# Kernel optimization log

Hardware: AMD Instinct MI355X
Metric: run time of the kernel (lower is better)

Reference implementation:

```python
import jax, jax.numpy as jnp
import numpy as np

B, T, H = 32, 64, 1024  # batch_size, input_number, hidden_size


def _lstm_cell(x, h, c, Wih, Whh, bih, bhh):
    # torch.nn.LSTMCell math: gate order i, f, g, o
    gates = x @ Wih.T + bih + h @ Whh.T + bhh
    i, f, g, o = jnp.split(gates, 4, axis=-1)
    c = jax.nn.sigmoid(f) * c + jax.nn.sigmoid(i) * jnp.tanh(g)
    h = jax.nn.sigmoid(o) * jnp.tanh(c)
    return h, c


def setup_inputs() -> dict:
    key = jax.random.key(0)
    ks = iter(jax.random.split(key, 64))

    def unif(shape, fan):
        s = 1.0 / np.sqrt(fan)
        return jax.random.uniform(next(ks), shape, jnp.float32, -s, s)

    inp = {
        'apperances': jax.random.normal(next(ks), (B, T, 2 * H), jnp.float32),
        'motions': jax.random.normal(next(ks), (B, T, 2 * H), jnp.float32),
    }
    # four LSTM cells: 1a/1m take 2H input, 2a/2m take H input
    for name, in_dim in [('1a', 2 * H), ('2a', H), ('1m', 2 * H), ('2m', H)]:
        inp['Wih_' + name] = unif((4 * H, in_dim), H)
        inp['Whh_' + name] = unif((4 * H, H), H)
        inp['bih_' + name] = unif((4 * H,), H)
        inp['bhh_' + name] = unif((4 * H,), H)
    # two-stream memory fusion (stand-in for MemoryRamTwoStreamModule)
    inp['Wg'] = unif((H, 2 * H), 2 * H)
    inp['bg'] = unif((H,), 2 * H)
    inp['Wa'] = unif((H, H), H)
    inp['ba'] = unif((H,), H)
    inp['Wm'] = unif((H, H), H)
    inp['bm'] = unif((H,), H)
    return inp


def reference(apperances, motions,
              Wih_1a, Whh_1a, bih_1a, bhh_1a,
              Wih_2a, Whh_2a, bih_2a, bhh_2a,
              Wih_1m, Whh_1m, bih_1m, bhh_1m,
              Wih_2m, Whh_2m, bih_2m, bhh_2m,
              Wg, bg, Wa, ba, Wm, bm):
    b, t, _ = apperances.shape
    h = Whh_1a.shape[1]
    xa = jnp.swapaxes(apperances, 0, 1)  # (T, B, 2H)
    xm = jnp.swapaxes(motions, 0, 1)     # (T, B, 2H)
    z = jnp.zeros((b, h), apperances.dtype)

    def step(carry, xs):
        h1a, c1a, h2a, c2a, h1m, c1m, h2m, c2m = carry
        xa_t, xm_t = xs
        h1m, c1m = _lstm_cell(xm_t, h1m, c1m, Wih_1m, Whh_1m, bih_1m, bhh_1m)
        h2m, c2m = _lstm_cell(h1m, h2m, c2m, Wih_2m, Whh_2m, bih_2m, bhh_2m)
        h1a, c1a = _lstm_cell(xa_t, h1a, c1a, Wih_1a, Whh_1a, bih_1a, bhh_1a)
        h2a, c2a = _lstm_cell(h1a, h2a, c2a, Wih_2a, Whh_2a, bih_2a, bhh_2a)
        return (h1a, c1a, h2a, c2a, h1m, c1m, h2m, c2m), (h2a, h2m)

    _, (Ha, Hm) = jax.lax.scan(step, (z, z, z, z, z, z, z, z), (xa, xm))
    Ha = jnp.swapaxes(Ha, 0, 1)  # (B, T, H)
    Hm = jnp.swapaxes(Hm, 0, 1)  # (B, T, H)
    # gated two-stream fusion per timestep (assumed MemoryRamTwoStreamModule)
    g = jax.nn.sigmoid(jnp.einsum('btk,hk->bth', jnp.concatenate([Ha, Hm], -1), Wg) + bg)
    mem = g * jnp.tanh(Ha @ Wa.T + ba) + (1.0 - g) * jnp.tanh(Hm @ Wm.T + bm)
    return mem  # (B, T, H)
```

## Files before the change

### kernel.cpp

```cpp
#include <hip/hip_runtime.h>
#include <cstdint>

typedef _Float16 f16;
typedef _Float16 f16x4v __attribute__((ext_vector_type(4)));
typedef _Float16 f16x8 __attribute__((ext_vector_type(8)));
typedef float f32x4 __attribute__((ext_vector_type(4)));

#define DEV static __device__ __forceinline__

#define GLDS16(gp, lp) __builtin_amdgcn_global_load_lds( \
    (const __attribute__((address_space(1))) void*)(gp), \
    (__attribute__((address_space(3))) void*)(lp), 16, 0, 0)

DEV float sigf(float x) { return 1.0f / (1.0f + __expf(-x)); }
DEV float tanh2(float x) {
  float e = __expf(-2.0f * fabsf(x));
  float t = (1.0f - e) / (1.0f + e);
  return x >= 0.0f ? t : -t;
}

DEV void waitflags(const unsigned* fp, int l) {
  unsigned f;
  do {
    f = __hip_atomic_load(fp + l, __ATOMIC_RELAXED, __HIP_MEMORY_SCOPE_AGENT);
  } while (__any(f == 0));
  asm volatile("" ::: "memory");
  __builtin_amdgcn_sched_barrier(0);
}

__global__ __launch_bounds__(256) void k_cvt_all(
    const float* __restrict__ s0, f16* __restrict__ d0,
    const float* __restrict__ s1, f16* __restrict__ d1,
    const float* __restrict__ s2, f16* __restrict__ d2,
    const float* __restrict__ s3, f16* __restrict__ d3,
    const float* __restrict__ s4, f16* __restrict__ d4,
    const float* __restrict__ s5, f16* __restrict__ d5,
    const float* __restrict__ s6, f16* __restrict__ d6) {
  int bid = blockIdx.x;
  const float* s; f16* d; int base;
  if (bid < 4096)       { s = s0; d = d0; base = bid; }
  else if (bid < 8192)  { s = s1; d = d1; base = bid - 4096; }
  else if (bid < 16384) { s = s2; d = d2; base = bid - 8192; }
  else if (bid < 24576) { s = s3; d = d3; base = bid - 16384; }
  else if (bid < 26624) { s = s4; d = d4; base = bid - 24576; }
  else if (bid < 27648) { s = s5; d = d5; base = bid - 26624; }
  else                  { s = s6; d = d6; base = bid - 27648; }
  int i = (base * 256 + threadIdx.x) * 4;
  float4 v = *(const float4*)(s + i);
  f16x4v o;
  o.x = (f16)v.x; o.y = (f16)v.y; o.z = (f16)v.z; o.w = (f16)v.w;
  *(f16x4v*)(d + i) = o;
}

__global__ __launch_bounds__(256) void k_packw1(const float* __restrict__ Wa,
                                                const float* __restrict__ Wm,
                                                f16* __restrict__ Pa,
                                                f16* __restrict__ Pm) {
  const float* W = blockIdx.y ? Wm : Wa;
  f16* P = blockIdx.y ? Pm : Pa;
  int i2 = blockIdx.x * 256 + threadIdx.x;
  int l = i2 & 63, frag = i2 >> 6;
  int kt = frag & 31, ug = frag >> 5;
  int gate = ug & 3, ut = ug >> 2;
  int row = gate * 1024 + ut * 16 + (l & 15);
  int k = kt * 32 + 8 * (l >> 4);
  const float* s = W + row * 1024 + k;
  f16x8 o;
#pragma unroll
  for (int j = 0; j < 8; ++j) o[j] = (f16)s[j];
  *(f16x8*)(P + frag * 512 + l * 8) = o;
}

__global__ __launch_bounds__(256) void k_packw2(const float* __restrict__ Wiha,
                                                const float* __restrict__ Whha,
                                                const float* __restrict__ Wihm,
                                                const float* __restrict__ Whhm,
                                                f16* __restrict__ Pa,
                                                f16* __restrict__ Pm) {
  const float* Wih = blockIdx.y ? Wihm : Wiha;
  const float* Whh = blockIdx.y ? Whhm : Whha;
  f16* P = blockIdx.y ? Pm : Pa;
  int i2 = blockIdx.x * 256 + threadIdx.x;
  int l = i2 & 63, frag = i2 >> 6;
  int kt = frag & 63, ug = frag >> 6;
  int gate = ug & 3, ut = ug >> 2;
  int row = gate * 1024 + ut * 16 + (l & 15);
  int k = kt * 32 + 8 * (l >> 4);
  const float* s = (k < 1024) ? (Wih + row * 1024 + k)
                              : (Whh + row * 1024 + (k - 1024));
  f16x8 o;
#pragma unroll
  for (int j = 0; j < 8; ++j) o[j] = (f16)s[j];
  *(f16x8*)(P + frag * 512 + l * 8) = o;
}

template <int NKT, int LDA>
__global__ __launch_bounds__(256) void k_igemm(
    const f16* __restrict__ A0, const f16* __restrict__ A1,
    const f16* __restrict__ B0, const f16* __restrict__ B1,
    const float* __restrict__ bi0, const float* __restrict__ bh0,
    const float* __restrict__ bi1, const float* __restrict__ bh1,
    f16* __restrict__ C0, f16* __restrict__ C1) {
  const f16* A = blockIdx.z ? A1 : A0;
  const f16* B = blockIdx.z ? B1 : B0;
  const float* bi = blockIdx.z ? bi1 : bi0;
  const float* bh = blockIdx.z ? bh1 : bh0;
  f16* C = blockIdx.z ? C1 : C0;

  __shared__ alignas(16) f16 As[128 * 64];
  __shared__ alignas(16) f16 Bs[128 * 64];

  int tid = threadIdx.x, l = tid & 63, w = tid >> 6;
  int m0 = blockIdx.x * 128, n0 = blockIdx.y * 128;
  int wm = (w & 1) * 64, wn = (w >> 1) * 64;
  int lr = l & 15, lg = l >> 4;
  int sr = w * 32 + (l >> 3);
  int sc = (l & 7) * 8;

  f32x4 acc[4][4];
  f32x4 zero = {0.f, 0.f, 0.f, 0.f};
#pragma unroll
  for (int mt = 0; mt < 4; ++mt)
#pragma unroll
    for (int nt = 0; nt < 4; ++nt) acc[mt][nt] = zero;

  for (int kt = 0; kt < NKT; ++kt) {
    int k0 = kt * 64;
#pragma unroll
    for (int c2 = 0; c2 < 4; ++c2) {
      GLDS16(A + (size_t)(m0 + sr + c2 * 8) * LDA + k0 + sc, &As[(w * 32 + c2 * 8) * 64]);
      GLDS16(B + (size_t)(n0 + sr + c2 * 8) * LDA + k0 + sc, &Bs[(w * 32 + c2 * 8) * 64]);
    }
    __syncthreads();
#pragma unroll
    for (int ks = 0; ks < 2; ++ks) {
      f16x8 af[4], bf[4];
#pragma unroll
      for (int mt = 0; mt < 4; ++mt)
        af[mt] = *(const f16x8*)&As[(wm + mt * 16 + lr) * 64 + ks * 32 + 8 * lg];
#pragma unroll
      for (int nt = 0; nt < 4; ++nt)
        bf[nt] = *(const f16x8*)&Bs[(wn + nt * 16 + lr) * 64 + ks * 32 + 8 * lg];
#pragma unroll
      for (int mt = 0; mt < 4; ++mt)
#pragma unroll
        for (int nt = 0; nt < 4; ++nt)
          acc[mt][nt] = __builtin_amdgcn_mfma_f32_16x16x32_f16(af[mt], bf[nt], acc[mt][nt], 0, 0, 0);
    }
    __syncthreads();
  }

#pragma unroll
  for (int nt = 0; nt < 4; ++nt) {
    int n = n0 + wn + nt * 16 + lr;
    float bsum = bi[n] + bh[n];
#pragma unroll
    for (int mt = 0; mt < 4; ++mt) {
      int m = m0 + wm + mt * 16 + lg * 4;
#pragma unroll
      for (int r = 0; r < 4; ++r)
        C[(size_t)(m + r) * 4096 + n] = (f16)(acc[mt][nt][r] + bsum);
    }
  }
}

__global__ __launch_bounds__(512, 1) void k_scan2(
    const f16* __restrict__ Wp1_a, const f16* __restrict__ Wp1_m,
    const f16* __restrict__ Wp2_a, const f16* __restrict__ Wp2_m,
    const f16* __restrict__ G_a, const f16* __restrict__ G_m,
    const float* __restrict__ bi2_a, const float* __restrict__ bh2_a,
    const float* __restrict__ bi2_m, const float* __restrict__ bh2_m,
    f16* __restrict__ H1h,
    f16* __restrict__ h2c,
    f16* __restrict__ HaHm,
    unsigned* __restrict__ flags1,
    unsigned* __restrict__ flags2) {
  int bi = blockIdx.x;
  int role = bi >> 7, s = (bi >> 6) & 1, ut = bi & 63, u0 = ut * 16;
  int tid = threadIdx.x, l = tid & 63, w = tid >> 6;
  int lr = l & 15, lg = l >> 4;
  const f16* G = s ? G_m : G_a;
  f16* H1s = H1h + (size_t)s * 64 * 32768;
  f16* h2s = h2c + (size_t)s * 64 * 32768;
  f16* H2o = HaHm + s * 1024;

  f16x8 wreg[8][4];
  if (role == 0) {
    const f16* Wp = s ? Wp1_m : Wp1_a;
#pragma unroll
    for (int ks = 0; ks < 4; ++ks)
#pragma unroll
      for (int g = 0; g < 4; ++g) {
        wreg[ks][g] = *(const f16x8*)(Wp + (size_t)((ut * 4 + g) * 32 + (w * 4 + ks)) * 512 + l * 8);
        asm volatile("" : "+v"(wreg[ks][g]));
      }
  } else {
    const f16* Wp = s ? Wp2_m : Wp2_a;
#pragma unroll
    for (int ks = 0; ks < 8; ++ks)
#pragma unroll
      for (int g = 0; g < 4; ++g) {
        wreg[ks][g] = *(const f16x8*)(Wp + (size_t)((ut * 4 + g) * 64 + (w * 8 + ks)) * 512 + l * 8);
        asm volatile("" : "+v"(wreg[ks][g]));
      }
  }

  __shared__ alignas(16) float red[8][64][33];
  __shared__ alignas(16) f16 Gs[32][4][16];

  int eb = tid >> 4, eu = tid & 15;
  int emt = eb >> 4, elg = (eb >> 2) & 3, er = eb & 3;
  int lred = elg * 16 + eu;
  int idxb = emt * 16 + er;
  float creg = 0.f;
  f32x4 zero = {0.f, 0.f, 0.f, 0.f};

  if (role == 0) {
    int pb = tid >> 4, pg2 = (tid >> 2) & 3, p4 = tid & 3;
    int cb = w * 128;
    for (int t = 0; t < 64; ++t) {
      f16x4v gfrag = *(const f16x4v*)(G + (size_t)(pb * 64 + t) * 4096 + pg2 * 1024 + u0 + p4 * 4);

      f32x4 acc[2][4];
#pragma unroll
      for (int mt = 0; mt < 2; ++mt)
#pragma unroll
        for (int g = 0; g < 4; ++g) acc[mt][g] = zero;

      if (t > 0) {
        if (w == 0) waitflags(flags1 + (size_t)(s * 64 + t - 1) * 64, l);
        __syncthreads();
        const f16* hp = H1s + (size_t)(t - 1) * 32768;
        f16x8 A0[4], A1[4];
#pragma unroll
        for (int ks = 0; ks < 4; ++ks) {
          int col = cb + ks * 32 + 8 * lg;
          A0[ks] = *(const f16x8*)(hp + lr * 1024 + col);
          A1[ks] = *(const f16x8*)(hp + (16 + lr) * 1024 + col);
        }
#pragma unroll
        for (int ks = 0; ks < 4; ++ks)
#pragma unroll
          for (int g = 0; g < 4; ++g) {
            acc[0][g] = __builtin_amdgcn_mfma_f32_16x16x32_f16(A0[ks], wreg[ks][g], acc[0][g], 0, 0, 0);
            acc[1][g] = __builtin_amdgcn_mfma_f32_16x16x32_f16(A1[ks], wreg[ks][g], acc[1][g], 0, 0, 0);
          }
      }

      *(f16x4v*)&Gs[pb][pg2][p4 * 4] = gfrag;
#pragma unroll
      for (int mt = 0; mt < 2; ++mt)
#pragma unroll
        for (int g = 0; g < 4; ++g)
#pragma unroll
          for (int r = 0; r < 4; ++r)
            red[w][l][(mt * 4 + g) * 4 + r] = acc[mt][g][r];
      __syncthreads();

      float pre[4];
#pragma unroll
      for (int g = 0; g < 4; ++g) {
        int idx = idxb + g * 4;
        pre[g] = red[0][lred][idx] + red[1][lred][idx] + red[2][lred][idx] +
                 red[3][lred][idx] + red[4][lred][idx] + red[5][lred][idx] +
                 red[6][lred][idx] + red[7][lred][idx] + (float)Gs[eb][g][eu];
      }
      float cn = sigf(pre[1]) * creg + sigf(pre[0]) * tanh2(pre[2]);
      creg = cn;
      union { unsigned short us; f16 h; } cv;
      cv.h = (f16)(sigf(pre[3]) * tanh2(cn));
      unsigned ov = (unsigned)__shfl_xor((int)(unsigned)cv.us, 1, 64);
      if (!(tid & 1)) {
        unsigned pkv = ((unsigned)cv.us) | (ov << 16);
        __hip_atomic_store((unsigned*)(H1s + (size_t)t * 32768 + eb * 1024 + u0 + eu), pkv,
                           __ATOMIC_RELAXED, __HIP_MEMORY_SCOPE_AGENT);
      }
      asm volatile("s_waitcnt vmcnt(0)" ::: "memory");
      __syncthreads();
      if (tid == 0)
        __hip_atomic_store(flags1 + (size_t)(s * 64 + t) * 64 + ut, 1u,
                           __ATOMIC_RELAXED, __HIP_MEMORY_SCOPE_AGENT);
    }
  } else {
    const float* bip = s ? bi2_m : bi2_a;
    const float* bhp = s ? bh2_m : bh2_a;
    float b2r[4];
#pragma unroll
    for (int g = 0; g < 4; ++g)
      b2r[g] = bip[g * 1024 + u0 + eu] + bhp[g * 1024 + u0 + eu];
    int cb = (w & 3) * 256;

    for (int t = 0; t < 64; ++t) {
      f32x4 acc[2][4];
#pragma unroll
      for (int mt = 0; mt < 2; ++mt)
#pragma unroll
        for (int g = 0; g < 4; ++g) acc[mt][g] = zero;

      if (w == 0) waitflags(flags1 + (size_t)(s * 64 + t) * 64, l);
      if (t > 0 && w == 4) waitflags(flags2 + (size_t)(s * 64 + t - 1) * 64, l);
      __syncthreads();

      if (w < 4) {
        const f16* hp = H1s + (size_t)t * 32768;
        f16x8 A0[4], A1[4], B0[4], B1[4];
#pragma unroll
        for (int ks = 0; ks < 4; ++ks) {
          int c0 = cb + ks * 32 + 8 * lg;
          int c1 = cb + (4 + ks) * 32 + 8 * lg;
          A0[ks] = *(const f16x8*)(hp + lr * 1024 + c0);
          A1[ks] = *(const f16x8*)(hp + (16 + lr) * 1024 + c0);
          B0[ks] = *(const f16x8*)(hp + lr * 1024 + c1);
          B1[ks] = *(const f16x8*)(hp + (16 + lr) * 1024 + c1);
        }
#pragma unroll
        for (int ks = 0; ks < 4; ++ks)
#pragma unroll
          for (int g = 0; g < 4; ++g) {
            acc[0][g] = __builtin_amdgcn_mfma_f32_16x16x32_f16(A0[ks], wreg[ks][g], acc[0][g], 0, 0, 0);
            acc[1][g] = __builtin_amdgcn_mfma_f32_16x16x32_f16(A1[ks], wreg[ks][g], acc[1][g], 0, 0, 0);
          }
#pragma unroll
        for (int ks = 0; ks < 4; ++ks)
#pragma unroll
          for (int g = 0; g < 4; ++g) {
            acc[0][g] = __builtin_amdgcn_mfma_f32_16x16x32_f16(B0[ks], wreg[4 + ks][g], acc[0][g], 0, 0, 0);
            acc[1][g] = __builtin_amdgcn_mfma_f32_16x16x32_f16(B1[ks], wreg[4 + ks][g], acc[1][g], 0, 0, 0);
          }
      } else if (t > 0) {
        const f16* hp = h2s + (size_t)(t - 1) * 32768;
        f16x8 A0[4], A1[4], B0[4], B1[4];
#pragma unroll
        for (int ks = 0; ks < 4; ++ks) {
          int c0 = cb + ks * 32 + 8 * lg;
          int c1 = cb + (4 + ks) * 32 + 8 * lg;
          A0[ks] = *(const f16x8*)(hp + lr * 1024 + c0);
          A1[ks] = *(const f16x8*)(hp + (16 + lr) * 1024 + c0);
          B0[ks] = *(const f16x8*)(hp + lr * 1024 + c1);
          B1[ks] = *(const f16x8*)(hp + (16 + lr) * 1024 + c1);
        }
#pragma unroll
        for (int ks = 0; ks < 4; ++ks)
#pragma unroll
          for (int g = 0; g < 4; ++g) {
            acc[0][g] = __builtin_amdgcn_mfma_f32_16x16x32_f16(A0[ks], wreg[ks][g], acc[0][g], 0, 0, 0);
            acc[1][g] = __builtin_amdgcn_mfma_f32_16x16x32_f16(A1[ks], wreg[ks][g], acc[1][g], 0, 0, 0);
          }
#pragma unroll
        for (int ks = 0; ks < 4; ++ks)
#pragma unroll
          for (int g = 0; g < 4; ++g) {
            acc[0][g] = __builtin_amdgcn_mfma_f32_16x16x32_f16(B0[ks], wreg[4 + ks][g], acc[0][g], 0, 0, 0);
            acc[1][g] = __builtin_amdgcn_mfma_f32_16x16x32_f16(B1[ks], wreg[4 + ks][g], acc[1][g], 0, 0, 0);
          }
      }

#pragma unroll
      for (int mt = 0; mt < 2; ++mt)
#pragma unroll
        for (int g = 0; g < 4; ++g)
#pragma unroll
          for (int r = 0; r < 4; ++r)
            red[w][l][(mt * 4 + g) * 4 + r] = acc[mt][g][r];
      __syncthreads();

      float pre[4];
#pragma unroll
      for (int g = 0; g < 4; ++g) {
        int idx = idxb + g * 4;
        pre[g] = red[0][lred][idx] + red[1][lred][idx] + red[2][lred][idx] +
                 red[3][lred][idx] + red[4][lred][idx] + red[5][lred][idx] +
                 red[6][lred][idx] + red[7][lred][idx] + b2r[g];
      }
      float cn = sigf(pre[1]) * creg + sigf(pre[0]) * tanh2(pre[2]);
      creg = cn;
      union { unsigned short us; f16 h; } cv;
      cv.h = (f16)(sigf(pre[3]) * tanh2(cn));
      unsigned ov = (unsigned)__shfl_xor((int)(unsigned)cv.us, 1, 64);
      if (!(tid & 1)) {
        unsigned pkv = ((unsigned)cv.us) | (ov << 16);
        __hip_atomic_store((unsigned*)(h2s + (size_t)t * 32768 + eb * 1024 + u0 + eu), pkv,
                           __ATOMIC_RELAXED, __HIP_MEMORY_SCOPE_AGENT);
        *(unsigned*)(H2o + (size_t)(eb * 64 + t) * 2048 + u0 + eu) = pkv;
      }
      asm volatile("s_waitcnt vmcnt(0)" ::: "memory");
      __syncthreads();
      if (tid == 0)
        __hip_atomic_store(flags2 + (size_t)(s * 64 + t) * 64 + ut, 1u,
                           __ATOMIC_RELAXED, __HIP_MEMORY_SCOPE_AGENT);
    }
  }
}

DEV void gemm_phase(const f16* __restrict__ H, int kA0,
                    const f16* __restrict__ Bp, int brs, int nk,
                    f16* As, f16* Bs, int m0, int n0, int w, int l,
                    int wm, int wn, f32x4 (&acc)[4][2]) {
  f32x4 zero = {0.f, 0.f, 0.f, 0.f};
#pragma unroll
  for (int mt = 0; mt < 4; ++mt)
#pragma unroll
    for (int nt = 0; nt < 2; ++nt) acc[mt][nt] = zero;
  int lr = l & 15, lg = l >> 4;
  int sc = (l & 7) * 8;
  for (int kt = 0; kt < nk; ++kt) {
    int ka = kA0 + kt * 64, kb = kt * 64;
#pragma unroll
    for (int c2 = 0; c2 < 4; ++c2)
      GLDS16(H + (size_t)(m0 + w * 32 + c2 * 8 + (l >> 3)) * 2048 + ka + sc,
             As + (w * 32 + c2 * 8) * 64);
#pragma unroll
    for (int c2 = 0; c2 < 2; ++c2)
      GLDS16(Bp + (size_t)(n0 + w * 16 + c2 * 8 + (l >> 3)) * brs + kb + sc,
             Bs + (w * 16 + c2 * 8) * 64);
    __syncthreads();
#pragma unroll
    for (int ks = 0; ks < 2; ++ks) {
      f16x8 af[4], bf[2];
#pragma unroll
      for (int mt = 0; mt < 4; ++mt)
        af[mt] = *(const f16x8*)&As[(wm + mt * 16 + lr) * 64 + ks * 32 + 8 * lg];
#pragma unroll
      for (int nt = 0; nt < 2; ++nt)
        bf[nt] = *(const f16x8*)&Bs[(wn + nt * 16 + lr) * 64 + ks * 32 + 8 * lg];
#pragma unroll
      for (int mt = 0; mt < 4; ++mt)
#pragma unroll
        for (int nt = 0; nt < 2; ++nt)
          acc[mt][nt] = __builtin_amdgcn_mfma_f32_16x16x32_f16(af[mt], bf[nt], acc[mt][nt], 0, 0, 0);
    }
    __syncthreads();
  }
}

__global__ __launch_bounds__(256) void k_fusion(
    const f16* __restrict__ H, const f16* __restrict__ Wg16,
    const f16* __restrict__ Wa16, const f16* __restrict__ Wm16,
    const float* __restrict__ bg, const float* __restrict__ ba,
    const float* __restrict__ bm, float* __restrict__ out) {
  __shared__ alignas(16) f16 As[128 * 64];
  __shared__ alignas(16) f16 Bs[64 * 64];
  int tid = threadIdx.x, l = tid & 63, w = tid >> 6;
  int m0 = blockIdx.x * 128, n0 = blockIdx.y * 64;
  int wm = (w & 1) * 64, wn = (w >> 1) * 32;
  int lr = l & 15, lg = l >> 4;

  f32x4 acc[4][2];
  float ta[4][2][4], tm[4][2][4];

  gemm_phase(H, 0, Wa16, 1024, 16, As, Bs, m0, n0, w, l, wm, wn, acc);
#pragma unroll
  for (int nt = 0; nt < 2; ++nt) {
    float bv = ba[n0 + wn + nt * 16 + lr];
#pragma unroll
    for (int mt = 0; mt < 4; ++mt)
#pragma unroll
      for (int r = 0; r < 4; ++r) ta[mt][nt][r] = tanh2(acc[mt][nt][r] + bv);
  }
  gemm_phase(H, 1024, Wm16, 1024, 16, As, Bs, m0, n0, w, l, wm, wn, acc);
#pragma unroll
  for (int nt = 0; nt < 2; ++nt) {
    float bv = bm[n0 + wn + nt * 16 + lr];
#pragma unroll
    for (int mt = 0; mt < 4; ++mt)
#pragma unroll
      for (int r = 0; r < 4; ++r) tm[mt][nt][r] = tanh2(acc[mt][nt][r] + bv);
  }
  gemm_phase(H, 0, Wg16, 2048, 32, As, Bs, m0, n0, w, l, wm, wn, acc);
#pragma unroll
  for (int nt = 0; nt < 2; ++nt) {
    int n = n0 + wn + nt * 16 + lr;
    float bv = bg[n];
#pragma unroll
    for (int mt = 0; mt < 4; ++mt) {
      int m = m0 + wm + mt * 16 + lg * 4;
#pragma unroll
      for (int r = 0; r < 4; ++r) {
        float g = sigf(acc[mt][nt][r] + bv);
        out[(size_t)(m + r) * 1024 + n] = tm[mt][nt][r] + g * (ta[mt][nt][r] - tm[mt][nt][r]);
      }
    }
  }
}

extern "C" void kernel_launch(void* const* d_in, const int* in_sizes, int n_in,
                              void* d_out, int out_size, void* d_ws, size_t ws_size,
                              hipStream_t stream) {
  const float* xa = (const float*)d_in[0];
  const float* xm = (const float*)d_in[1];
  const float* Wih_1a = (const float*)d_in[2];
  const float* Whh_1a = (const float*)d_in[3];
  const float* bih_1a = (const float*)d_in[4];
  const float* bhh_1a = (const float*)d_in[5];
  const float* Wih_2a = (const float*)d_in[6];
  const float* Whh_2a = (const float*)d_in[7];
  const float* bih_2a = (const float*)d_in[8];
  const float* bhh_2a = (const float*)d_in[9];
  const float* Wih_1m = (const float*)d_in[10];
  const float* Whh_1m = (const float*)d_in[11];
  const float* bih_1m = (const float*)d_in[12];
  const float* bhh_1m = (const float*)d_in[13];
  const float* Wih_2m = (const float*)d_in[14];
  const float* Whh_2m = (const float*)d_in[15];
  const float* bih_2m = (const float*)d_in[16];
  const float* bhh_2m = (const float*)d_in[17];
  const float* Wg = (const float*)d_in[18];
  const float* bg = (const float*)d_in[19];
  const float* Wa = (const float*)d_in[20];
  const float* ba = (const float*)d_in[21];
  const float* Wm = (const float*)d_in[22];
  const float* bm = (const float*)d_in[23];

  char* ws = (char*)d_ws;
  const size_t MB = 1024ull * 1024;
  if (ws_size < 138 * MB) return;

  f16* x16a    = (f16*)(ws + 0 * MB);
  f16* x16m    = (f16*)(ws + 8 * MB);
  f16* W1ih16a = (f16*)(ws + 16 * MB);
  f16* W1ih16m = (f16*)(ws + 32 * MB);
  f16* W1p_a   = (f16*)(ws + 48 * MB);
  f16* W1p_m   = (f16*)(ws + 56 * MB);
  f16* W2p_a   = (f16*)(ws + 64 * MB);
  f16* W2p_m   = (f16*)(ws + 80 * MB);
  f16* Wg16    = (f16*)(ws + 96 * MB);
  f16* Wa16    = (f16*)(ws + 100 * MB);
  f16* Wm16    = (f16*)(ws + 102 * MB);
  f16* G0a     = (f16*)(ws + 104 * MB);
  f16* G0m     = (f16*)(ws + 120 * MB);
  unsigned* flags1 = (unsigned*)(ws + 136 * MB);
  unsigned* flags2 = (unsigned*)(ws + 136 * MB + 32768);
  f16* HaHm    = (f16*)(ws + 0 * MB);
  f16* H1h     = (f16*)(ws + 8 * MB);
  f16* h2c     = (f16*)(ws + 16 * MB);

  dim3 B256(256);
  k_cvt_all<<<28672, B256, 0, stream>>>(xa, x16a, xm, x16m, Wih_1a, W1ih16a,
                                        Wih_1m, W1ih16m, Wg, Wg16, Wa, Wa16,
                                        Wm, Wm16);
  k_packw1<<<dim3(2048, 2), B256, 0, stream>>>(Whh_1a, Whh_1m, W1p_a, W1p_m);
  k_packw2<<<dim3(4096, 2), B256, 0, stream>>>(Wih_2a, Whh_2a, Wih_2m, Whh_2m,
                                               W2p_a, W2p_m);
  hipMemsetAsync(flags1, 0, 65536, stream);

  k_igemm<32, 2048><<<dim3(16, 32, 2), B256, 0, stream>>>(
      x16a, x16m, W1ih16a, W1ih16m, bih_1a, bhh_1a, bih_1m, bhh_1m, G0a, G0m);

  k_scan2<<<256, dim3(512), 0, stream>>>(
      W1p_a, W1p_m, W2p_a, W2p_m, G0a, G0m,
      bih_2a, bhh_2a, bih_2m, bhh_2m, H1h, h2c, HaHm, flags1, flags2);

  k_fusion<<<dim3(16, 16), B256, 0, stream>>>(HaHm, Wg16, Wa16, Wm16, bg, ba,
                                              bm, (float*)d_out);
}
```

Baseline: 729.8 us.

## Fuse layer-1 input GEMM into scan kernel with per-timestep readiness counters

Removes the separate input-projection GEMM launch and runs it inside the persistent scan kernel on 128 extra blocks. Those blocks publish per-timestep-pair counters, and the layer-1 scan blocks poll the counters so the recurrence can start before the whole projection is finished. The input is converted and transposed to time-major order so each timestep's rows are contiguous, and the Wih fp32 weights are converted to fp16 on the fly instead of by a separate pass. Layer-2 output is written once to HaHm in time-major order, which drops the duplicate h2 buffer, and the fusion kernel remaps rows on output. The trade-offs are more spin-waiting, a GEMM with smaller tiles that loads fp32 weights directly, and reliance on all 384 blocks being co-resident.

```diff
diff --git a/kernel.cpp b/kernel.cpp
--- a/kernel.cpp
+++ b/kernel.cpp
@@ -28,28 +28,39 @@
   __builtin_amdgcn_sched_barrier(0);
 }
 
+DEV void waitcnt_ge(const unsigned* cp, unsigned want) {
+  unsigned c;
+  do {
+    c = __hip_atomic_load(cp, __ATOMIC_RELAXED, __HIP_MEMORY_SCOPE_AGENT);
+  } while (__any(c < want));
+  asm volatile("" ::: "memory");
+  __builtin_amdgcn_sched_barrier(0);
+}
+
 __global__ __launch_bounds__(256) void k_cvt_all(
     const float* __restrict__ s0, f16* __restrict__ d0,
     const float* __restrict__ s1, f16* __restrict__ d1,
     const float* __restrict__ s2, f16* __restrict__ d2,
     const float* __restrict__ s3, f16* __restrict__ d3,
-    const float* __restrict__ s4, f16* __restrict__ d4,
-    const float* __restrict__ s5, f16* __restrict__ d5,
-    const float* __restrict__ s6, f16* __restrict__ d6) {
+    const float* __restrict__ s4, f16* __restrict__ d4) {
   int bid = blockIdx.x;
-  const float* s; f16* d; int base;
-  if (bid < 4096)       { s = s0; d = d0; base = bid; }
-  else if (bid < 8192)  { s = s1; d = d1; base = bid - 4096; }
-  else if (bid < 16384) { s = s2; d = d2; base = bid - 8192; }
-  else if (bid < 24576) { s = s3; d = d3; base = bid - 16384; }
-  else if (bid < 26624) { s = s4; d = d4; base = bid - 24576; }
-  else if (bid < 27648) { s = s5; d = d5; base = bid - 26624; }
-  else                  { s = s6; d = d6; base = bid - 27648; }
+  const float* s; f16* d; int base; int xpose = 0;
+  if (bid < 4096)       { s = s0; d = d0; base = bid; xpose = 1; }
+  else if (bid < 8192)  { s = s1; d = d1; base = bid - 4096; xpose = 1; }
+  else if (bid < 10240) { s = s2; d = d2; base = bid - 8192; }
+  else if (bid < 11264) { s = s3; d = d3; base = bid - 10240; }
+  else                  { s = s4; d = d4; base = bid - 11264; }
   int i = (base * 256 + threadIdx.x) * 4;
   float4 v = *(const float4*)(s + i);
   f16x4v o;
   o.x = (f16)v.x; o.y = (f16)v.y; o.z = (f16)v.z; o.w = (f16)v.w;
-  *(f16x4v*)(d + i) = o;
+  if (xpose) {
+    int row = i >> 11, c = i & 2047;
+    int orow = ((row & 63) << 5) | (row >> 6);
+    *(f16x4v*)(d + (size_t)orow * 2048 + c) = o;
+  } else {
+    *(f16x4v*)(d + i) = o;
+  }
 }
 
 __global__ __launch_bounds__(256) void k_packw1(const float* __restrict__ Wa,
@@ -94,94 +105,127 @@
   *(f16x8*)(P + frag * 512 + l * 8) = o;
 }
 
-template <int NKT, int LDA>
-__global__ __launch_bounds__(256) void k_igemm(
-    const f16* __restrict__ A0, const f16* __restrict__ A1,
-    const f16* __restrict__ B0, const f16* __restrict__ B1,
-    const float* __restrict__ bi0, const float* __restrict__ bh0,
-    const float* __restrict__ bi1, const float* __restrict__ bh1,
-    f16* __restrict__ C0, f16* __restrict__ C1) {
-  const f16* A = blockIdx.z ? A1 : A0;
-  const f16* B = blockIdx.z ? B1 : B0;
-  const float* bi = blockIdx.z ? bi1 : bi0;
-  const float* bh = blockIdx.z ? bh1 : bh0;
-  f16* C = blockIdx.z ? C1 : C0;
-
-  __shared__ alignas(16) f16 As[128 * 64];
-  __shared__ alignas(16) f16 Bs[128 * 64];
-
-  int tid = threadIdx.x, l = tid & 63, w = tid >> 6;
-  int m0 = blockIdx.x * 128, n0 = blockIdx.y * 128;
-  int wm = (w & 1) * 64, wn = (w >> 1) * 64;
-  int lr = l & 15, lg = l >> 4;
-  int sr = w * 32 + (l >> 3);
-  int sc = (l & 7) * 8;
-
-  f32x4 acc[4][4];
-  f32x4 zero = {0.f, 0.f, 0.f, 0.f};
-#pragma unroll
-  for (int mt = 0; mt < 4; ++mt)
-#pragma unroll
-    for (int nt = 0; nt < 4; ++nt) acc[mt][nt] = zero;
-
-  for (int kt = 0; kt < NKT; ++kt) {
-    int k0 = kt * 64;
-#pragma unroll
-    for (int c2 = 0; c2 < 4; ++c2) {
-      GLDS16(A + (size_t)(m0 + sr + c2 * 8) * LDA + k0 + sc, &As[(w * 32 + c2 * 8) * 64]);
-      GLDS16(B + (size_t)(n0 + sr + c2 * 8) * LDA + k0 + sc, &Bs[(w * 32 + c2 * 8) * 64]);
-    }
-    __syncthreads();
-#pragma unroll
-    for (int ks = 0; ks < 2; ++ks) {
-      f16x8 af[4], bf[4];
-#pragma unroll
-      for (int mt = 0; mt < 4; ++mt)
-        af[mt] = *(const f16x8*)&As[(wm + mt * 16 + lr) * 64 + ks * 32 + 8 * lg];
-#pragma unroll
-      for (int nt = 0; nt < 4; ++nt)
-        bf[nt] = *(const f16x8*)&Bs[(wn + nt * 16 + lr) * 64 + ks * 32 + 8 * lg];
-#pragma unroll
-      for (int mt = 0; mt < 4; ++mt)
-#pragma unroll
-        for (int nt = 0; nt < 4; ++nt)
-          acc[mt][nt] = __builtin_amdgcn_mfma_f32_16x16x32_f16(af[mt], bf[nt], acc[mt][nt], 0, 0, 0);
-    }
-    __syncthreads();
-  }
-
-#pragma unroll
-  for (int nt = 0; nt < 4; ++nt) {
-    int n = n0 + wn + nt * 16 + lr;
-    float bsum = bi[n] + bh[n];
-#pragma unroll
-    for (int mt = 0; mt < 4; ++mt) {
-      int m = m0 + wm + mt * 16 + lg * 4;
-#pragma unroll
-      for (int r = 0; r < 4; ++r)
-        C[(size_t)(m + r) * 4096 + n] = (f16)(acc[mt][nt][r] + bsum);
-    }
-  }
-}
+struct ScanSm { float red[8][64][33]; f16 Gs[32][4][16]; };
+struct GemmSm { f16 As[2][64 * 64]; f16 Bs[2][128 * 64]; };
 
 __global__ __launch_bounds__(512, 1) void k_scan2(
     const f16* __restrict__ Wp1_a, const f16* __restrict__ Wp1_m,
     const f16* __restrict__ Wp2_a, const f16* __restrict__ Wp2_m,
-    const f16* __restrict__ G_a, const f16* __restrict__ G_m,
+    const f16* __restrict__ xt_a, const f16* __restrict__ xt_m,
+    const float* __restrict__ W1f_a, const float* __restrict__ W1f_m,
+    const float* __restrict__ bi1_a, const float* __restrict__ bh1_a,
+    const float* __restrict__ bi1_m, const float* __restrict__ bh1_m,
     const float* __restrict__ bi2_a, const float* __restrict__ bh2_a,
     const float* __restrict__ bi2_m, const float* __restrict__ bh2_m,
+    f16* __restrict__ G0a, f16* __restrict__ G0m,
     f16* __restrict__ H1h,
-    f16* __restrict__ h2c,
     f16* __restrict__ HaHm,
     unsigned* __restrict__ flags1,
-    unsigned* __restrict__ flags2) {
+    unsigned* __restrict__ flags2,
+    unsigned* __restrict__ gcnt) {
   int bi = blockIdx.x;
-  int role = bi >> 7, s = (bi >> 6) & 1, ut = bi & 63, u0 = ut * 16;
   int tid = threadIdx.x, l = tid & 63, w = tid >> 6;
   int lr = l & 15, lg = l >> 4;
-  const f16* G = s ? G_m : G_a;
+  __shared__ alignas(16) char smem[sizeof(ScanSm)];
+
+  if (bi < 128) {
+    GemmSm* gs = (GemmSm*)smem;
+    int g2 = w >> 2;
+    int tid2 = tid & 255;
+    int w4 = tid2 >> 6;
+    f16* As = gs->As[g2];
+    f16* Bs = gs->Bs[g2];
+    int wm4 = (w4 >> 1) * 32, wn4 = (w4 & 1) * 64;
+    int sc = (l & 7) * 8;
+    int br = tid2 >> 1, bh = tid2 & 1;
+    for (int r2 = 0; r2 < 8; ++r2) {
+      int job = r2 * 256 + bi * 2 + g2;
+      int mt_ = job >> 6, rem = job & 63;
+      int sj = rem >> 5, ntile = rem & 31;
+      const f16* A = sj ? xt_m : xt_a;
+      const float* Bw = sj ? W1f_m : W1f_a;
+      const float* b1i = sj ? bi1_m : bi1_a;
+      const float* b1h = sj ? bh1_m : bh1_a;
+      f16* C = sj ? G0m : G0a;
+      int m0 = mt_ * 64, n0 = ntile * 128;
+
+      f32x4 acc[2][4];
+      f32x4 zero = {0.f, 0.f, 0.f, 0.f};
+#pragma unroll
+      for (int mt = 0; mt < 2; ++mt)
+#pragma unroll
+        for (int nt = 0; nt < 4; ++nt) acc[mt][nt] = zero;
+
+      for (int kt = 0; kt < 32; ++kt) {
+        int k0 = kt * 64;
+#pragma unroll
+        for (int c2 = 0; c2 < 2; ++c2)
+          GLDS16(A + (size_t)(m0 + w4 * 16 + c2 * 8 + (l >> 3)) * 2048 + k0 + sc,
+                 As + (w4 * 16 + c2 * 8) * 64);
+        float4 bv[8];
+#pragma unroll
+        for (int j = 0; j < 8; ++j)
+          bv[j] = *(const float4*)(Bw + (size_t)(n0 + br) * 2048 + k0 + bh * 32 + j * 4);
+#pragma unroll
+        for (int j = 0; j < 8; ++j) {
+          f16x4v c4;
+          c4.x = (f16)bv[j].x; c4.y = (f16)bv[j].y;
+          c4.z = (f16)bv[j].z; c4.w = (f16)bv[j].w;
+          *(f16x4v*)(Bs + br * 64 + bh * 32 + j * 4) = c4;
+        }
+        __syncthreads();
+#pragma unroll
+        for (int ks = 0; ks < 2; ++ks) {
+          f16x8 af[2], bf[4];
+#pragma unroll
+          for (int mt = 0; mt < 2; ++mt)
+            af[mt] = *(const f16x8*)&As[(wm4 + mt * 16 + lr) * 64 + ks * 32 + 8 * lg];
+#pragma unroll
+          for (int nt = 0; nt < 4; ++nt)
+            bf[nt] = *(const f16x8*)&Bs[(wn4 + nt * 16 + lr) * 64 + ks * 32 + 8 * lg];
+#pragma unroll
+          for (int mt = 0; mt < 2; ++mt)
+#pragma unroll
+            for (int nt = 0; nt < 4; ++nt)
+              acc[mt][nt] = __builtin_amdgcn_mfma_f32_16x16x32_f16(af[mt], bf[nt], acc[mt][nt], 0, 0, 0);
+        }
+        __syncthreads();
+      }
+#pragma unroll
+      for (int nt = 0; nt < 4; ++nt) {
+        int n = n0 + wn4 + nt * 16 + lr;
+        float bsum = b1i[n] + b1h[n];
+#pragma unroll
+        for (int mt = 0; mt < 2; ++mt) {
+          int m = m0 + wm4 + mt * 16 + lg * 4;
+#pragma unroll
+          for (int r = 0; r < 4; ++r) {
+            union { unsigned short us; f16 h; } cv;
+            cv.h = (f16)(acc[mt][nt][r] + bsum);
+            unsigned ov = (unsigned)__shfl_xor((int)(unsigned)cv.us, 1, 64);
+            if (!(l & 1)) {
+              unsigned pkv = ((unsigned)cv.us) | (ov << 16);
+              __hip_atomic_store((unsigned*)(C + (size_t)(m + r) * 4096 + n), pkv,
+                                 __ATOMIC_RELAXED, __HIP_MEMORY_SCOPE_AGENT);
+            }
+          }
+        }
+      }
+      asm volatile("s_waitcnt vmcnt(0)" ::: "memory");
+      __syncthreads();
+      if (tid == 0 || tid == 256)
+        __hip_atomic_fetch_add(&gcnt[sj * 32 + mt_], 1u, __ATOMIC_RELAXED,
+                               __HIP_MEMORY_SCOPE_AGENT);
+    }
+    return;
+  }
+
+  ScanSm* ss = (ScanSm*)smem;
+  int role = (bi >= 256);
+  int idx = bi - (role ? 256 : 128);
+  int s = idx >> 6, ut = idx & 63, u0 = ut * 16;
+  const f16* G = s ? G0m : G0a;
   f16* H1s = H1h + (size_t)s * 64 * 32768;
-  f16* h2s = h2c + (size_t)s * 64 * 32768;
   f16* H2o = HaHm + s * 1024;
 
   f16x8 wreg[8][4];
@@ -204,9 +248,6 @@
         asm volatile("" : "+v"(wreg[ks][g]));
       }
   }
-
-  __shared__ alignas(16) float red[8][64][33];
-  __shared__ alignas(16) f16 Gs[32][4][16];
 
   int eb = tid >> 4, eu = tid & 15;
   int emt = eb >> 4, elg = (eb >> 2) & 3, er = eb & 3;
@@ -219,7 +260,13 @@
     int pb = tid >> 4, pg2 = (tid >> 2) & 3, p4 = tid & 3;
     int cb = w * 128;
     for (int t = 0; t < 64; ++t) {
-      f16x4v gfrag = *(const f16x4v*)(G + (size_t)(pb * 64 + t) * 4096 + pg2 * 1024 + u0 + p4 * 4);
+      if (w == 0) {
+        waitcnt_ge(&gcnt[s * 32 + (t >> 1)], 32u);
+        if (t > 0) waitflags(flags1 + (size_t)(s * 64 + t - 1) * 64, l);
+      }
+      __syncthreads();
+
+      f16x4v gfrag = *(const f16x4v*)(G + (size_t)(t * 32 + pb) * 4096 + pg2 * 1024 + u0 + p4 * 4);
 
       f32x4 acc[2][4];
 #pragma unroll
@@ -228,8 +275,6 @@
         for (int g = 0; g < 4; ++g) acc[mt][g] = zero;
 
       if (t > 0) {
-        if (w == 0) waitflags(flags1 + (size_t)(s * 64 + t - 1) * 64, l);
-        __syncthreads();
         const f16* hp = H1s + (size_t)(t - 1) * 32768;
         f16x8 A0[4], A1[4];
 #pragma unroll
@@ -247,23 +292,25 @@
           }
       }
 
-      *(f16x4v*)&Gs[pb][pg2][p4 * 4] = gfrag;
+      *(f16x4v*)&ss->Gs[pb][pg2][p4 * 4] = gfrag;
 #pragma unroll
       for (int mt = 0; mt < 2; ++mt)
 #pragma unroll
         for (int g = 0; g < 4; ++g)
 #pragma unroll
           for (int r = 0; r < 4; ++r)
-            red[w][l][(mt * 4 + g) * 4 + r] = acc[mt][g][r];
+            ss->red[w][l][(mt * 4 + g) * 4 + r] = acc[mt][g][r];
       __syncthreads();
 
       float pre[4];
 #pragma unroll
       for (int g = 0; g < 4; ++g) {
-        int idx = idxb + g * 4;
-        pre[g] = red[0][lred][idx] + red[1][lred][idx] + red[2][lred][idx] +
-                 red[3][lred][idx] + red[4][lred][idx] + red[5][lred][idx] +
-                 red[6][lred][idx] + red[7][lred][idx] + (float)Gs[eb][g][eu];
+        int idx2 = idxb + g * 4;
+        pre[g] = ss->red[0][lred][idx2] + ss->red[1][lred][idx2] +
+                 ss->red[2][lred][idx2] + ss->red[3][lred][idx2] +
+                 ss->red[4][lred][idx2] + ss->red[5][lred][idx2] +
+                 ss->red[6][lred][idx2] + ss->red[7][lred][idx2] +
+                 (float)ss->Gs[eb][g][eu];
       }
       float cn = sigf(pre[1]) * creg + sigf(pre[0]) * tanh2(pre[2]);
       creg = cn;
@@ -328,16 +375,16 @@
             acc[1][g] = __builtin_amdgcn_mfma_f32_16x16x32_f16(B1[ks], wreg[4 + ks][g], acc[1][g], 0, 0, 0);
           }
       } else if (t > 0) {
-        const f16* hp = h2s + (size_t)(t - 1) * 32768;
+        const f16* hp = HaHm + (size_t)((t - 1) * 32) * 2048 + s * 1024;
         f16x8 A0[4], A1[4], B0[4], B1[4];
 #pragma unroll
         for (int ks = 0; ks < 4; ++ks) {
           int c0 = cb + ks * 32 + 8 * lg;
           int c1 = cb + (4 + ks) * 32 + 8 * lg;
-          A0[ks] = *(const f16x8*)(hp + lr * 1024 + c0);
-          A1[ks] = *(const f16x8*)(hp + (16 + lr) * 1024 + c0);
-          B0[ks] = *(const f16x8*)(hp + lr * 1024 + c1);
-          B1[ks] = *(const f16x8*)(hp + (16 + lr) * 1024 + c1);
+          A0[ks] = *(const f16x8*)(hp + (size_t)lr * 2048 + c0);
+          A1[ks] = *(const f16x8*)(hp + (size_t)(16 + lr) * 2048 + c0);
+          B0[ks] = *(const f16x8*)(hp + (size_t)lr * 2048 + c1);
+          B1[ks] = *(const f16x8*)(hp + (size_t)(16 + lr) * 2048 + c1);
         }
 #pragma unroll
         for (int ks = 0; ks < 4; ++ks)
@@ -361,16 +408,17 @@
         for (int g = 0; g < 4; ++g)
 #pragma unroll
           for (int r = 0; r < 4; ++r)
-            red[w][l][(mt * 4 + g) * 4 + r] = acc[mt][g][r];
+            ss->red[w][l][(mt * 4 + g) * 4 + r] = acc[mt][g][r];
       __syncthreads();
 
       float pre[4];
 #pragma unroll
       for (int g = 0; g < 4; ++g) {
-        int idx = idxb + g * 4;
-        pre[g] = red[0][lred][idx] + red[1][lred][idx] + red[2][lred][idx] +
-                 red[3][lred][idx] + red[4][lred][idx] + red[5][lred][idx] +
-                 red[6][lred][idx] + red[7][lred][idx] + b2r[g];
+        int idx2 = idxb + g * 4;
+        pre[g] = ss->red[0][lred][idx2] + ss->red[1][lred][idx2] +
+                 ss->red[2][lred][idx2] + ss->red[3][lred][idx2] +
+                 ss->red[4][lred][idx2] + ss->red[5][lred][idx2] +
+                 ss->red[6][lred][idx2] + ss->red[7][lred][idx2] + b2r[g];
       }
       float cn = sigf(pre[1]) * creg + sigf(pre[0]) * tanh2(pre[2]);
       creg = cn;
@@ -379,9 +427,8 @@
       unsigned ov = (unsigned)__shfl_xor((int)(unsigned)cv.us, 1, 64);
       if (!(tid & 1)) {
         unsigned pkv = ((unsigned)cv.us) | (ov << 16);
-        __hip_atomic_store((unsigned*)(h2s + (size_t)t * 32768 + eb * 1024 + u0 + eu), pkv,
+        __hip_atomic_store((unsigned*)(H2o + (size_t)(t * 32 + eb) * 2048 + u0 + eu), pkv,
                            __ATOMIC_RELAXED, __HIP_MEMORY_SCOPE_AGENT);
-        *(unsigned*)(H2o + (size_t)(eb * 64 + t) * 2048 + u0 + eu) = pkv;
       }
       asm volatile("s_waitcnt vmcnt(0)" ::: "memory");
       __syncthreads();
@@ -477,7 +524,9 @@
 #pragma unroll
       for (int r = 0; r < 4; ++r) {
         float g = sigf(acc[mt][nt][r] + bv);
-        out[(size_t)(m + r) * 1024 + n] = tm[mt][nt][r] + g * (ta[mt][nt][r] - tm[mt][nt][r]);
+        int mr = m + r;
+        size_t orow = (size_t)((mr & 31) * 64 + (mr >> 5));
+        out[orow * 1024 + n] = tm[mt][nt][r] + g * (ta[mt][nt][r] - tm[mt][nt][r]);
       }
     }
   }
@@ -515,40 +564,36 @@
   const size_t MB = 1024ull * 1024;
   if (ws_size < 138 * MB) return;
 
-  f16* x16a    = (f16*)(ws + 0 * MB);
-  f16* x16m    = (f16*)(ws + 8 * MB);
-  f16* W1ih16a = (f16*)(ws + 16 * MB);
-  f16* W1ih16m = (f16*)(ws + 32 * MB);
-  f16* W1p_a   = (f16*)(ws + 48 * MB);
-  f16* W1p_m   = (f16*)(ws + 56 * MB);
-  f16* W2p_a   = (f16*)(ws + 64 * MB);
-  f16* W2p_m   = (f16*)(ws + 80 * MB);
-  f16* Wg16    = (f16*)(ws + 96 * MB);
-  f16* Wa16    = (f16*)(ws + 100 * MB);
-  f16* Wm16    = (f16*)(ws + 102 * MB);
-  f16* G0a     = (f16*)(ws + 104 * MB);
-  f16* G0m     = (f16*)(ws + 120 * MB);
-  unsigned* flags1 = (unsigned*)(ws + 136 * MB);
-  unsigned* flags2 = (unsigned*)(ws + 136 * MB + 32768);
-  f16* HaHm    = (f16*)(ws + 0 * MB);
-  f16* H1h     = (f16*)(ws + 8 * MB);
-  f16* h2c     = (f16*)(ws + 16 * MB);
+  f16* xt_a  = (f16*)(ws + 0 * MB);
+  f16* xt_m  = (f16*)(ws + 8 * MB);
+  f16* W1p_a = (f16*)(ws + 16 * MB);
+  f16* W1p_m = (f16*)(ws + 24 * MB);
+  f16* W2p_a = (f16*)(ws + 32 * MB);
+  f16* W2p_m = (f16*)(ws + 48 * MB);
+  f16* Wg16  = (f16*)(ws + 64 * MB);
+  f16* Wa16  = (f16*)(ws + 68 * MB);
+  f16* Wm16  = (f16*)(ws + 70 * MB);
+  f16* G0a   = (f16*)(ws + 72 * MB);
+  f16* G0m   = (f16*)(ws + 88 * MB);
+  f16* H1h   = (f16*)(ws + 104 * MB);
+  f16* HaHm  = (f16*)(ws + 112 * MB);
+  unsigned* flags1 = (unsigned*)(ws + 120 * MB);
+  unsigned* flags2 = (unsigned*)(ws + 120 * MB + 32768);
+  unsigned* gcnt   = (unsigned*)(ws + 120 * MB + 65536);
 
   dim3 B256(256);
-  k_cvt_all<<<28672, B256, 0, stream>>>(xa, x16a, xm, x16m, Wih_1a, W1ih16a,
-                                        Wih_1m, W1ih16m, Wg, Wg16, Wa, Wa16,
+  k_cvt_all<<<12288, B256, 0, stream>>>(xa, xt_a, xm, xt_m, Wg, Wg16, Wa, Wa16,
                                         Wm, Wm16);
   k_packw1<<<dim3(2048, 2), B256, 0, stream>>>(Whh_1a, Whh_1m, W1p_a, W1p_m);
   k_packw2<<<dim3(4096, 2), B256, 0, stream>>>(Wih_2a, Whh_2a, Wih_2m, Whh_2m,
                                                W2p_a, W2p_m);
-  hipMemsetAsync(flags1, 0, 65536, stream);
-
-  k_igemm<32, 2048><<<dim3(16, 32, 2), B256, 0, stream>>>(
-      x16a, x16m, W1ih16a, W1ih16m, bih_1a, bhh_1a, bih_1m, bhh_1m, G0a, G0m);
-
-  k_scan2<<<256, dim3(512), 0, stream>>>(
-      W1p_a, W1p_m, W2p_a, W2p_m, G0a, G0m,
-      bih_2a, bhh_2a, bih_2m, bhh_2m, H1h, h2c, HaHm, flags1, flags2);
+  hipMemsetAsync(flags1, 0, 131072, stream);
+
+  k_scan2<<<384, dim3(512), 0, stream>>>(
+      W1p_a, W1p_m, W2p_a, W2p_m, xt_a, xt_m, Wih_1a, Wih_1m,
+      bih_1a, bhh_1a, bih_1m, bhh_1m,
+      bih_2a, bhh_2a, bih_2m, bhh_2m,
+      G0a, G0m, H1h, HaHm, flags1, flags2, gcnt);
 
   k_fusion<<<dim3(16, 16), B256, 0, stream>>>(HaHm, Wg16, Wa16, Wm16, bg, ba,
                                               bm, (float*)d_out);
```

New measurement: 1.448 ms. 1.98x slower.
